# Kernel tuning notes

Hardware: AMD Instinct MI355X
Metric: run time of the kernel (lower is better)

The kernel has to match this reference:

```python
import jax, jax.numpy as jnp
import numpy as np

H = 56; W = 56; WS = 7; SHIFT = 3; HEADS = 4; C = 128; B = 64
N = WS * WS            # 49 tokens per window
NW = (H // WS) * (W // WS)  # 64 windows per image
HD = C // HEADS
EPS = 1e-5


def _rel_index():
    # matches get_relative_index: pairwise coord diffs in [-(WS-1), WS-1];
    # torch negative indexing wraps, so take mod (2*WS-1)
    coords = np.array([[i, j] for i in range(WS) for j in range(WS)])
    rel = coords[None, :, :] - coords[:, None, :]          # (N, N, 2)
    return (rel % (2 * WS - 1)).astype(np.int32)


def _attn_mask():
    # matches get_attn_mask for shifted windows
    img = np.zeros((H, W))
    sl = (slice(0, -WS), slice(-WS, -SHIFT), slice(-SHIFT, None))
    cnt = 0
    for hs in sl:
        for ws_ in sl:
            img[hs, ws_] = cnt
            cnt += 1
    m = img.reshape(H // WS, WS, W // WS, WS).transpose(0, 2, 1, 3).reshape(NW, N)
    am = m[:, None, :] - m[:, :, None]                     # (NW, N, N)
    return np.where(am != 0, -100.0, 0.0).astype(np.float32)

_REL_IDX = _rel_index()
_MASK = _attn_mask()


def _layernorm(x, g, b):
    mu = jnp.mean(x, axis=-1, keepdims=True)
    var = jnp.mean(jnp.square(x - mu), axis=-1, keepdims=True)
    return (x - mu) * jax.lax.rsqrt(var + EPS) * g + b


def setup_inputs() -> dict:
    key = jax.random.key(0)
    ks = jax.random.split(key, 16)
    s = 0.02
    return {
        "x": jax.random.normal(ks[0], (B, H * W, C), jnp.float32),
        "wq": jax.random.normal(ks[1], (C, C), jnp.float32) * s,
        "bq": jnp.zeros((C,), jnp.float32),
        "wk": jax.random.normal(ks[2], (C, C), jnp.float32) * s,
        "bk": jnp.zeros((C,), jnp.float32),
        "wv": jax.random.normal(ks[3], (C, C), jnp.float32) * s,
        "bv": jnp.zeros((C,), jnp.float32),
        "wo": jax.random.normal(ks[4], (C, C), jnp.float32) * s,
        "bo": jnp.zeros((C,), jnp.float32),
        "rel_table": jax.random.normal(ks[5], (2 * WS - 1, 2 * WS - 1, HEADS), jnp.float32) * s,
        "ln1_g": jnp.ones((C,), jnp.float32),
        "ln1_b": jnp.zeros((C,), jnp.float32),
        "ln2_g": jnp.ones((C,), jnp.float32),
        "ln2_b": jnp.zeros((C,), jnp.float32),
        "w1": jax.random.normal(ks[6], (C, 4 * C), jnp.float32) * s,
        "b1": jnp.zeros((4 * C,), jnp.float32),
        "w2": jax.random.normal(ks[7], (4 * C, C), jnp.float32) * s,
        "b2": jnp.zeros((C,), jnp.float32),
    }


def reference(x, wq, bq, wk, bk, wv, bv, wo, bo, rel_table,
              ln1_g, ln1_b, ln2_g, ln2_b, w1, b1, w2, b2):
    shortcut = x                                     # (B, H*W, C)
    h = _layernorm(x, ln1_g, ln1_b).reshape(B, H, W, C)
    h = jnp.roll(h, (-SHIFT, -SHIFT), axis=(1, 2))   # cyclic shift
    # window partition -> (B*NW, N, C)
    h = h.reshape(B, H // WS, WS, W // WS, WS, C).transpose(0, 1, 3, 2, 4, 5)
    h = h.reshape(B * NW, N, C)
    q = (h @ wq + bq).reshape(B * NW, N, HEADS, HD)
    k = (h @ wk + bk).reshape(B * NW, N, HEADS, HD)
    v = (h @ wv + bv).reshape(B * NW, N, HEADS, HD)
    attn = jnp.einsum('nqhd,nkhd->nhqk', q, k) / np.sqrt(HD).astype(np.float32)
    bias = rel_table[_REL_IDX[:, :, 0], _REL_IDX[:, :, 1]]  # (N, N, HEADS)
    attn = attn + jnp.transpose(bias, (2, 0, 1))[None]      # (1, H, N, N)
    # shifted-window additive mask
    attn = attn.reshape(B, NW, HEADS, N, N) + jnp.asarray(_MASK)[None, :, None]
    attn = jax.nn.softmax(attn.reshape(B * NW, HEADS, N, N), axis=-1)
    out = jnp.einsum('nhqk,nkhd->nqhd', attn, v).reshape(B * NW, N, C)
    out = out @ wo + bo
    # faithful to source bug: output taken directly from window-ordered tokens
    h = out.reshape(B, H * W, C)
    h = h + shortcut
    m = _layernorm(h, ln2_g, ln2_b)
    m = jax.nn.gelu(m @ w1 + b1, approximate=False) @ w2 + b2
    return h + m
```

## Files before the change

### kernel.cpp

```cpp
#include <hip/hip_runtime.h>

typedef __attribute__((ext_vector_type(8))) short short8;
typedef __attribute__((ext_vector_type(4))) float f32x4;
typedef unsigned short u16;
typedef unsigned int u32;

#define MFMA16(a, b, c) __builtin_amdgcn_mfma_f32_16x16x32_bf16((a), (b), (c), 0, 0, 0)
#define SCALE_Q 0.1767766952966369f
#define TOKENS 200704

__device__ __forceinline__ u16 f2bf(float x) {
  u32 u = __float_as_uint(x);
  u32 r = u + 0x7FFF + ((u >> 16) & 1);
  return (u16)(r >> 16);
}

__device__ __forceinline__ float gelu_f(float x) {
  float u = 0.7978845608f * (x + 0.044715f * x * x * x);
  float e = __expf(2.f * u);
  float t = 1.f - 2.f / (e + 1.f);
  return 0.5f * x * (1.f + t);
}

__device__ __forceinline__ u32 pairpack(u16 me, int lane) {
  u32 pv = (u32)__shfl_xor((int)me, 1);
  return (u32)me | (pv << 16);
}

__global__ __launch_bounds__(256) void k0_weights(
    const float* __restrict__ wq, const float* __restrict__ wk, const float* __restrict__ wv,
    const float* __restrict__ wo, const float* __restrict__ w1, const float* __restrict__ w2,
    const float* __restrict__ bq, const float* __restrict__ bk, const float* __restrict__ bv,
    u16* __restrict__ wqkvt, u16* __restrict__ wot, u16* __restrict__ w1t, u16* __restrict__ w2t,
    float* __restrict__ bqkv) {
  int idx = blockIdx.x * 256 + threadIdx.x;
  if (idx < 49152) {
    int n = idx >> 7, k = idx & 127;
    float v;
    if (n < 128) v = wq[k * 128 + n] * SCALE_Q;
    else if (n < 256) v = wk[k * 128 + (n - 128)];
    else v = wv[k * 128 + (n - 256)];
    wqkvt[idx] = f2bf(v);
  } else if (idx < 65536) {
    int j = idx - 49152;
    int n = j >> 7, k = j & 127;
    wot[j] = f2bf(wo[k * 128 + n]);
  } else if (idx < 131072) {
    int j = idx - 65536;
    int n = j >> 7, k = j & 127;
    w1t[j] = f2bf(w1[k * 512 + n]);
  } else if (idx < 196608) {
    int j = idx - 131072;
    int n = j >> 9, k = j & 511;
    w2t[j] = f2bf(w2[k * 128 + n]);
  } else if (idx < 196992) {
    int n = idx - 196608;
    float v;
    if (n < 128) v = bq[n] * SCALE_Q;
    else if (n < 256) v = bk[n - 128];
    else v = bv[n - 256];
    bqkv[n] = v;
  }
}

__global__ __launch_bounds__(256) void k0_biasmask(const float* __restrict__ rel, float* __restrict__ bm) {
  int idx = blockIdx.x * 256 + threadIdx.x;
  int reg = idx & 3;
  int lane = (idx >> 2) & 63;
  int nt = (idx >> 8) & 3;
  int mt = (idx >> 10) & 3;
  int h = (idx >> 12) & 3;
  int wi = idx >> 14;
  int r = mt * 16 + ((lane >> 4) << 2) + reg;
  int c = nt * 16 + (lane & 15);
  float v = -1e30f;
  if (r < 49 && c < 49) {
    int qr = r / 7, qc = r % 7, kr = c / 7, kc = c % 7;
    int i0 = (kr - qr + 13) % 13, i1 = (kc - qc + 13) % 13;
    v = rel[(i0 * 13 + i1) * 4 + h];
    int gh = (wi >> 3) * 7 + qr, gw = (wi & 7) * 7 + qc;
    int kh = (wi >> 3) * 7 + kr, kw = (wi & 7) * 7 + kc;
    int rq = (gh < 49 ? 0 : (gh < 53 ? 1 : 2)) * 3 + (gw < 49 ? 0 : (gw < 53 ? 1 : 2));
    int rk = (kh < 49 ? 0 : (kh < 53 ? 1 : 2)) * 3 + (kw < 49 ? 0 : (kw < 53 ? 1 : 2));
    if (rq != rk) v -= 100.f;
  }
  bm[idx] = v;
}

__global__ __launch_bounds__(256) void k1_ln1(const float* __restrict__ x, const float* __restrict__ g,
                                              const float* __restrict__ b, u16* __restrict__ hwin) {
  int wid = threadIdx.x >> 6, lane = threadIdx.x & 63;
  int t = blockIdx.x * 4 + wid;
  float2 v = *(const float2*)(x + (size_t)t * 128 + lane * 2);
  float s = v.x + v.y;
#pragma unroll
  for (int o = 1; o < 64; o <<= 1) s += __shfl_xor(s, o);
  float mu = s * 0.0078125f;
  float dx = v.x - mu, dy = v.y - mu;
  float q = dx * dx + dy * dy;
#pragma unroll
  for (int o = 1; o < 64; o <<= 1) q += __shfl_xor(q, o);
  float rstd = rsqrtf(q * 0.0078125f + 1e-5f);
  float y0 = dx * rstd * g[lane * 2] + b[lane * 2];
  float y1 = dy * rstd * g[lane * 2 + 1] + b[lane * 2 + 1];
  int bi = t / 3136, hw = t - bi * 3136;
  int oh = hw / 56, ow = hw - oh * 56;
  int gh = oh - 3; if (gh < 0) gh += 56;
  int gw = ow - 3; if (gw < 0) gw += 56;
  int win = bi * 64 + (gh / 7) * 8 + gw / 7;
  int n = (gh % 7) * 7 + (gw % 7);
  u32 packed = (u32)f2bf(y0) | ((u32)f2bf(y1) << 16);
  *(u32*)(hwin + (size_t)(win * 49 + n) * 128 + lane * 2) = packed;
}

__global__ __launch_bounds__(256) void k2_qkv(const u16* __restrict__ hwin, const u16* __restrict__ wt,
                                              const float* __restrict__ bqkv, u16* __restrict__ qb,
                                              u16* __restrict__ kb, u16* __restrict__ vb) {
  int tid = threadIdx.x, lane = tid & 63, w = tid >> 6;
  int g = lane >> 4, l15 = lane & 15;
  int row0 = blockIdx.x * 128 + w * 32;
  short8 a[2][4];
#pragma unroll
  for (int mt = 0; mt < 2; ++mt)
#pragma unroll
    for (int kt = 0; kt < 4; ++kt)
      a[mt][kt] = *(const short8*)(hwin + (size_t)(row0 + mt * 16 + l15) * 128 + kt * 32 + g * 8);
  const f32x4 vz = {0.f, 0.f, 0.f, 0.f};
  for (int nb = 0; nb < 6; ++nb) {
    f32x4 acc[2][4];
#pragma unroll
    for (int i = 0; i < 2; ++i)
#pragma unroll
      for (int j = 0; j < 4; ++j) acc[i][j] = vz;
#pragma unroll
    for (int kt = 0; kt < 4; ++kt) {
      short8 bfr[4];
#pragma unroll
      for (int nt = 0; nt < 4; ++nt)
        bfr[nt] = *(const short8*)(wt + (size_t)(nb * 64 + nt * 16 + l15) * 128 + kt * 32 + g * 8);
#pragma unroll
      for (int mt = 0; mt < 2; ++mt)
#pragma unroll
        for (int nt = 0; nt < 4; ++nt) acc[mt][nt] = MFMA16(a[mt][kt], bfr[nt], acc[mt][nt]);
    }
    u16* dst; int cb;
    if (nb < 2) { dst = qb; cb = nb * 64; }
    else if (nb < 4) { dst = kb; cb = (nb - 2) * 64; }
    else { dst = vb; cb = (nb - 4) * 64; }
#pragma unroll
    for (int mt = 0; mt < 2; ++mt)
#pragma unroll
      for (int nt = 0; nt < 4; ++nt) {
        int c = cb + nt * 16 + l15;
        float bias = bqkv[nb * 64 + nt * 16 + l15];
#pragma unroll
        for (int reg = 0; reg < 4; ++reg) {
          int token = row0 + mt * 16 + g * 4 + reg;
          u16 me = f2bf(acc[mt][nt][reg] + bias);
          u32 word = pairpack(me, lane);
          if (!(lane & 1)) *(u32*)(dst + (size_t)token * 128 + c) = word;
        }
      }
  }
}

__global__ __launch_bounds__(256) void k3_attn(const u16* __restrict__ qb, const u16* __restrict__ kb,
                                               const u16* __restrict__ vb, const float* __restrict__ bm,
                                               const u16* __restrict__ wot, const float* __restrict__ bo,
                                               const float* __restrict__ x, const float* __restrict__ g2,
                                               const float* __restrict__ b2, float* __restrict__ dout,
                                               u16* __restrict__ ln2) {
  __shared__ u16 smem[16384 + 8192];
  u16* pl = smem;
  u16* vtl = smem + 16384;
  u16* aol = smem;
  int win = blockIdx.x;
  int tid = threadIdx.x;
  int lane = tid & 63, head = tid >> 6;
  int g = lane >> 4, l15 = lane & 15;

  {
    int t = tid >> 2, dq = tid & 3;
    long grow = (long)win * 49 + t;
    bool valid = (t < 49) && (grow < TOKENS);
    short8 r[4];
#pragma unroll
    for (int c = 0; c < 4; ++c) {
      if (valid) r[c] = *(const short8*)(vb + grow * 128 + dq * 32 + c * 8);
      else r[c] = short8{0, 0, 0, 0, 0, 0, 0, 0};
    }
#pragma unroll
    for (int c = 0; c < 4; ++c)
#pragma unroll
      for (int e = 0; e < 8; ++e) {
        int d = dq * 32 + c * 8 + e;
        int byte_ = (d * 128 + t * 2) ^ ((((d & 7) ^ ((d >> 3) & 7))) << 4);
        *(u16*)((char*)vtl + byte_) = (u16)r[c][e];
      }
  }

  u16* myp = pl + head * 4096;
  short8 aq[4], bk_[4];
#pragma unroll
  for (int mt = 0; mt < 4; ++mt)
    aq[mt] = *(const short8*)(qb + (size_t)(win * 49 + mt * 16 + l15) * 128 + head * 32 + g * 8);
#pragma unroll
  for (int nt = 0; nt < 4; ++nt)
    bk_[nt] = *(const short8*)(kb + (size_t)(win * 49 + nt * 16 + l15) * 128 + head * 32 + g * 8);
  const f32x4* bmv = (const f32x4*)bm + ((win & 63) * 4 + head) * 1024;
  f32x4 s[4][4];
#pragma unroll
  for (int mt = 0; mt < 4; ++mt)
#pragma unroll
    for (int nt = 0; nt < 4; ++nt) s[mt][nt] = bmv[(mt * 4 + nt) * 64 + lane];
#pragma unroll
  for (int mt = 0; mt < 4; ++mt)
#pragma unroll
    for (int nt = 0; nt < 4; ++nt) s[mt][nt] = MFMA16(aq[mt], bk_[nt], s[mt][nt]);
#pragma unroll
  for (int mt = 0; mt < 4; ++mt)
#pragma unroll
    for (int reg = 0; reg < 4; ++reg) {
      float m = fmaxf(fmaxf(s[mt][0][reg], s[mt][1][reg]), fmaxf(s[mt][2][reg], s[mt][3][reg]));
#pragma unroll
      for (int o = 1; o < 16; o <<= 1) m = fmaxf(m, __shfl_xor(m, o));
      float p0 = __expf(s[mt][0][reg] - m);
      float p1 = __expf(s[mt][1][reg] - m);
      float p2 = __expf(s[mt][2][reg] - m);
      float p3 = __expf(s[mt][3][reg] - m);
      float sum = p0 + p1 + p2 + p3;
#pragma unroll
      for (int o = 1; o < 16; o <<= 1) sum += __shfl_xor(sum, o);
      float rinv = 1.f / sum;
      s[mt][0][reg] = p0 * rinv; s[mt][1][reg] = p1 * rinv;
      s[mt][2][reg] = p2 * rinv; s[mt][3][reg] = p3 * rinv;
    }
#pragma unroll
  for (int mt = 0; mt < 4; ++mt)
#pragma unroll
    for (int nt = 0; nt < 4; ++nt)
#pragma unroll
      for (int reg = 0; reg < 4; ++reg) {
        int r = mt * 16 + g * 4 + reg, c = nt * 16 + l15;
        int byte_ = ((r << 7) + (c << 1)) ^ ((r & 7) << 4);
        *(u16*)((char*)myp + byte_) = f2bf(s[mt][nt][reg]);
      }
  __syncthreads();

  short8 vf[2][2];
#pragma unroll
  for (int kk = 0; kk < 2; ++kk)
#pragma unroll
    for (int n2 = 0; n2 < 2; ++n2) {
      int d = head * 32 + n2 * 16 + l15;
      int byte_ = (d * 128 + (kk * 32 + g * 8) * 2) ^ ((((d & 7) ^ ((d >> 3) & 7))) << 4);
      vf[kk][n2] = *(const short8*)((const char*)vtl + byte_);
    }
  const f32x4 vz = {0.f, 0.f, 0.f, 0.f};
  f32x4 o[4][2];
#pragma unroll
  for (int mt = 0; mt < 4; ++mt) { o[mt][0] = vz; o[mt][1] = vz; }
#pragma unroll
  for (int mt = 0; mt < 4; ++mt)
#pragma unroll
    for (int kk = 0; kk < 2; ++kk) {
      int r = mt * 16 + l15;
      int byte_ = ((r << 7) + kk * 64 + g * 16) ^ ((r & 7) << 4);
      short8 pa = *(const short8*)((const char*)myp + byte_);
#pragma unroll
      for (int n2 = 0; n2 < 2; ++n2) o[mt][n2] = MFMA16(pa, vf[kk][n2], o[mt][n2]);
    }
  __syncthreads();

#pragma unroll
  for (int mt = 0; mt < 4; ++mt)
#pragma unroll
    for (int n2 = 0; n2 < 2; ++n2)
#pragma unroll
      for (int reg = 0; reg < 4; ++reg) {
        int r = mt * 16 + g * 4 + reg, c = head * 32 + n2 * 16 + l15;
        u16 me = f2bf(o[mt][n2][reg]);
        u32 word = pairpack(me, lane);
        if (!(lane & 1)) {
          int byte_ = ((r << 8) + c * 2) ^ ((r & 7) << 4);
          *(u32*)((char*)aol + byte_) = word;
        }
      }
  __syncthreads();

  int w = head;
  f32x4 pacc[8];
#pragma unroll
  for (int nt = 0; nt < 8; ++nt) pacc[nt] = vz;
#pragma unroll
  for (int kt = 0; kt < 4; ++kt) {
    int row = w * 16 + l15;
    int byte_ = ((row << 8) + kt * 64 + g * 16) ^ ((row & 7) << 4);
    short8 af = *(const short8*)((const char*)aol + byte_);
#pragma unroll
    for (int nt = 0; nt < 8; ++nt) {
      short8 bf = *(const short8*)(wot + (size_t)(nt * 16 + l15) * 128 + kt * 32 + g * 8);
      pacc[nt] = MFMA16(af, bf, pacc[nt]);
    }
  }
#pragma unroll
  for (int reg = 0; reg < 4; ++reg) {
    int row = w * 16 + g * 4 + reg;
    if (row < 49) {
      size_t token = (size_t)win * 49 + row;
      float hv[8];
      float s1 = 0.f, s2 = 0.f;
#pragma unroll
      for (int nt = 0; nt < 8; ++nt) {
        int c = nt * 16 + l15;
        float v = pacc[nt][reg] + bo[c] + x[token * 128 + c];
        dout[token * 128 + c] = v;
        hv[nt] = v; s1 += v; s2 += v * v;
      }
#pragma unroll
      for (int o = 1; o < 16; o <<= 1) { s1 += __shfl_xor(s1, o); s2 += __shfl_xor(s2, o); }
      float mu = s1 * 0.0078125f;
      float rstd = rsqrtf(fmaxf(s2 * 0.0078125f - mu * mu, 0.f) + 1e-5f);
#pragma unroll
      for (int nt = 0; nt < 8; ++nt) {
        int c = nt * 16 + l15;
        u16 me = f2bf((hv[nt] - mu) * rstd * g2[c] + b2[c]);
        u32 word = pairpack(me, lane);
        if (!(lane & 1)) *(u32*)(ln2 + token * 128 + c) = word;
      }
    }
  }
}

__global__ __launch_bounds__(256) void k5_mlp(const u16* __restrict__ ln2, const u16* __restrict__ w1t,
                                              const float* __restrict__ b1, const u16* __restrict__ w2t,
                                              const float* __restrict__ b2, float* __restrict__ dout) {
  __shared__ u16 h1[64 * 512];
  int tid = threadIdx.x, lane = tid & 63, w = tid >> 6;
  int g = lane >> 4, l15 = lane & 15;
  int row0 = blockIdx.x * 64;
  const f32x4 vz = {0.f, 0.f, 0.f, 0.f};

  {
    int r0 = w * 16;
    short8 a[4];
#pragma unroll
    for (int kt = 0; kt < 4; ++kt)
      a[kt] = *(const short8*)(ln2 + (size_t)(row0 + r0 + l15) * 128 + kt * 32 + g * 8);
    for (int nb = 0; nb < 8; ++nb) {
      f32x4 acc[4];
#pragma unroll
      for (int j = 0; j < 4; ++j) acc[j] = vz;
#pragma unroll
      for (int kt = 0; kt < 4; ++kt) {
        short8 bf[4];
#pragma unroll
        for (int nt = 0; nt < 4; ++nt)
          bf[nt] = *(const short8*)(w1t + (size_t)(nb * 64 + nt * 16 + l15) * 128 + kt * 32 + g * 8);
#pragma unroll
        for (int nt = 0; nt < 4; ++nt) acc[nt] = MFMA16(a[kt], bf[nt], acc[nt]);
      }
#pragma unroll
      for (int nt = 0; nt < 4; ++nt) {
        float bias = b1[nb * 64 + nt * 16 + l15];
#pragma unroll
        for (int reg = 0; reg < 4; ++reg) {
          int r = r0 + g * 4 + reg;
          int c = nb * 64 + nt * 16 + l15;
          u16 me = f2bf(gelu_f(acc[nt][reg] + bias));
          u32 word = pairpack(me, lane);
          if (!(lane & 1)) {
            int byte_ = (r * 1024 + c * 2) ^ ((r & 7) << 4);
            *(u32*)((char*)h1 + byte_) = word;
          }
        }
      }
    }
  }
  __syncthreads();

  {
    int c0 = w * 32;
    f32x4 acc2[4][2];
#pragma unroll
    for (int i = 0; i < 4; ++i) { acc2[i][0] = vz; acc2[i][1] = vz; }
#pragma unroll
    for (int kt = 0; kt < 16; ++kt) {
      short8 bf[2];
#pragma unroll
      for (int n2 = 0; n2 < 2; ++n2)
        bf[n2] = *(const short8*)(w2t + (size_t)(c0 + n2 * 16 + l15) * 512 + kt * 32 + g * 8);
#pragma unroll
      for (int mt = 0; mt < 4; ++mt) {
        int r = mt * 16 + l15;
        int byte_ = (r * 1024 + kt * 64 + g * 16) ^ ((r & 7) << 4);
        short8 af = *(const short8*)((const char*)h1 + byte_);
#pragma unroll
        for (int n2 = 0; n2 < 2; ++n2) acc2[mt][n2] = MFMA16(af, bf[n2], acc2[mt][n2]);
      }
    }
#pragma unroll
    for (int mt = 0; mt < 4; ++mt)
#pragma unroll
      for (int n2 = 0; n2 < 2; ++n2) {
        int c = c0 + n2 * 16 + l15;
        float bias = b2[c];
#pragma unroll
        for (int reg = 0; reg < 4; ++reg) {
          size_t token = (size_t)row0 + mt * 16 + g * 4 + reg;
          size_t i = token * 128 + c;
          dout[i] = acc2[mt][n2][reg] + bias + dout[i];
        }
      }
  }
}

extern "C" void kernel_launch(void* const* d_in, const int* in_sizes, int n_in,
                              void* d_out, int out_size, void* d_ws, size_t ws_size,
                              hipStream_t stream) {
  const float* x    = (const float*)d_in[0];
  const float* wq   = (const float*)d_in[1];
  const float* bq   = (const float*)d_in[2];
  const float* wk   = (const float*)d_in[3];
  const float* bk   = (const float*)d_in[4];
  const float* wv   = (const float*)d_in[5];
  const float* bv   = (const float*)d_in[6];
  const float* wo   = (const float*)d_in[7];
  const float* bo   = (const float*)d_in[8];
  const float* rel  = (const float*)d_in[9];
  const float* ln1g = (const float*)d_in[10];
  const float* ln1b = (const float*)d_in[11];
  const float* ln2g = (const float*)d_in[12];
  const float* ln2b = (const float*)d_in[13];
  const float* w1   = (const float*)d_in[14];
  const float* b1   = (const float*)d_in[15];
  const float* w2   = (const float*)d_in[16];
  const float* b2   = (const float*)d_in[17];
  float* out = (float*)d_out;
  char* ws = (char*)d_ws;

  float* bmask = (float*)(ws);
  u16* wqkvt = (u16*)(ws + (size_t)(4 << 20));
  u16* wot   = (u16*)(ws + (size_t)(4 << 20) + 196608);
  u16* w1t   = (u16*)(ws + (size_t)(4 << 20) + 229376);
  u16* w2t   = (u16*)(ws + (size_t)(4 << 20) + 360448);
  float* bqkv = (float*)(ws + (size_t)(4 << 20) + 491520);
  const size_t SB = (size_t)TOKENS * 128 * 2;
  u16* hwin = (u16*)(ws + (size_t)(8 << 20));
  u16* qb   = (u16*)(ws + (size_t)(8 << 20) + SB);
  u16* kb   = (u16*)(ws + (size_t)(8 << 20) + 2 * SB);
  u16* vb   = (u16*)(ws + (size_t)(8 << 20) + 3 * SB);
  u16* ln2  = hwin;

  k0_weights<<<770, 256, 0, stream>>>(wq, wk, wv, wo, w1, w2, bq, bk, bv,
                                      wqkvt, wot, w1t, w2t, bqkv);
  k0_biasmask<<<4096, 256, 0, stream>>>(rel, bmask);
  k1_ln1<<<50176, 256, 0, stream>>>(x, ln1g, ln1b, hwin);
  k2_qkv<<<1568, 256, 0, stream>>>(hwin, wqkvt, bqkv, qb, kb, vb);
  k3_attn<<<4096, 256, 0, stream>>>(qb, kb, vb, bmask, wot, bo, x, ln2g, ln2b, out, ln2);
  k5_mlp<<<3136, 256, 0, stream>>>(ln2, w1t, b1, w2t, b2, out);
}
```

Baseline: 884.3 us.

## Halve per-block rows in QKV and MLP kernels, store bf16 directly to LDS

The QKV projection now gives each wave 16 rows instead of 32 and launches twice as many blocks. The MLP kernel handles 32 rows per block, splitting the hidden columns across wave pairs, which halves its shared-memory tile and doubles the grid. Shared-memory epilogue writes in attention and MLP replace the shuffle-based pair packing with plain 16-bit stores. This aims to cut registers and LDS per block for higher occupancy and fewer shuffles, at the cost of more weight reloads per token and narrower LDS writes.

```diff
diff --git a/kernel.cpp b/kernel.cpp
--- a/kernel.cpp
+++ b/kernel.cpp
@@ -118,20 +118,16 @@
                                               u16* __restrict__ kb, u16* __restrict__ vb) {
   int tid = threadIdx.x, lane = tid & 63, w = tid >> 6;
   int g = lane >> 4, l15 = lane & 15;
-  int row0 = blockIdx.x * 128 + w * 32;
-  short8 a[2][4];
-#pragma unroll
-  for (int mt = 0; mt < 2; ++mt)
-#pragma unroll
-    for (int kt = 0; kt < 4; ++kt)
-      a[mt][kt] = *(const short8*)(hwin + (size_t)(row0 + mt * 16 + l15) * 128 + kt * 32 + g * 8);
+  int row0 = blockIdx.x * 64 + w * 16;
+  short8 a[4];
+#pragma unroll
+  for (int kt = 0; kt < 4; ++kt)
+    a[kt] = *(const short8*)(hwin + (size_t)(row0 + l15) * 128 + kt * 32 + g * 8);
   const f32x4 vz = {0.f, 0.f, 0.f, 0.f};
   for (int nb = 0; nb < 6; ++nb) {
-    f32x4 acc[2][4];
-#pragma unroll
-    for (int i = 0; i < 2; ++i)
-#pragma unroll
-      for (int j = 0; j < 4; ++j) acc[i][j] = vz;
+    f32x4 acc[4];
+#pragma unroll
+    for (int j = 0; j < 4; ++j) acc[j] = vz;
 #pragma unroll
     for (int kt = 0; kt < 4; ++kt) {
       short8 bfr[4];
@@ -139,28 +135,24 @@
       for (int nt = 0; nt < 4; ++nt)
         bfr[nt] = *(const short8*)(wt + (size_t)(nb * 64 + nt * 16 + l15) * 128 + kt * 32 + g * 8);
 #pragma unroll
-      for (int mt = 0; mt < 2; ++mt)
-#pragma unroll
-        for (int nt = 0; nt < 4; ++nt) acc[mt][nt] = MFMA16(a[mt][kt], bfr[nt], acc[mt][nt]);
+      for (int nt = 0; nt < 4; ++nt) acc[nt] = MFMA16(a[kt], bfr[nt], acc[nt]);
     }
     u16* dst; int cb;
     if (nb < 2) { dst = qb; cb = nb * 64; }
     else if (nb < 4) { dst = kb; cb = (nb - 2) * 64; }
     else { dst = vb; cb = (nb - 4) * 64; }
 #pragma unroll
-    for (int mt = 0; mt < 2; ++mt)
-#pragma unroll
-      for (int nt = 0; nt < 4; ++nt) {
-        int c = cb + nt * 16 + l15;
-        float bias = bqkv[nb * 64 + nt * 16 + l15];
-#pragma unroll
-        for (int reg = 0; reg < 4; ++reg) {
-          int token = row0 + mt * 16 + g * 4 + reg;
-          u16 me = f2bf(acc[mt][nt][reg] + bias);
-          u32 word = pairpack(me, lane);
-          if (!(lane & 1)) *(u32*)(dst + (size_t)token * 128 + c) = word;
-        }
-      }
+    for (int nt = 0; nt < 4; ++nt) {
+      int c = cb + nt * 16 + l15;
+      float bias = bqkv[nb * 64 + nt * 16 + l15];
+#pragma unroll
+      for (int reg = 0; reg < 4; ++reg) {
+        int token = row0 + g * 4 + reg;
+        u16 me = f2bf(acc[nt][reg] + bias);
+        u32 word = pairpack(me, lane);
+        if (!(lane & 1)) *(u32*)(dst + (size_t)token * 128 + c) = word;
+      }
+    }
   }
 }
 
@@ -279,12 +271,8 @@
 #pragma unroll
       for (int reg = 0; reg < 4; ++reg) {
         int r = mt * 16 + g * 4 + reg, c = head * 32 + n2 * 16 + l15;
-        u16 me = f2bf(o[mt][n2][reg]);
-        u32 word = pairpack(me, lane);
-        if (!(lane & 1)) {
-          int byte_ = ((r << 8) + c * 2) ^ ((r & 7) << 4);
-          *(u32*)((char*)aol + byte_) = word;
-        }
+        int byte_ = ((r << 8) + c * 2) ^ ((r & 7) << 4);
+        *(u16*)((char*)aol + byte_) = f2bf(o[mt][n2][reg]);
       }
   __syncthreads();
 
@@ -335,19 +323,20 @@
 __global__ __launch_bounds__(256) void k5_mlp(const u16* __restrict__ ln2, const u16* __restrict__ w1t,
                                               const float* __restrict__ b1, const u16* __restrict__ w2t,
                                               const float* __restrict__ b2, float* __restrict__ dout) {
-  __shared__ u16 h1[64 * 512];
+  __shared__ u16 h1[32 * 512];
   int tid = threadIdx.x, lane = tid & 63, w = tid >> 6;
   int g = lane >> 4, l15 = lane & 15;
-  int row0 = blockIdx.x * 64;
+  int row0 = blockIdx.x * 32;
   const f32x4 vz = {0.f, 0.f, 0.f, 0.f};
 
   {
-    int r0 = w * 16;
+    int r0 = (w & 1) * 16, c0 = (w >> 1) * 256;
     short8 a[4];
 #pragma unroll
     for (int kt = 0; kt < 4; ++kt)
       a[kt] = *(const short8*)(ln2 + (size_t)(row0 + r0 + l15) * 128 + kt * 32 + g * 8);
-    for (int nb = 0; nb < 8; ++nb) {
+#pragma unroll
+    for (int nb = 0; nb < 4; ++nb) {
       f32x4 acc[4];
 #pragma unroll
       for (int j = 0; j < 4; ++j) acc[j] = vz;
@@ -356,23 +345,20 @@
         short8 bf[4];
 #pragma unroll
         for (int nt = 0; nt < 4; ++nt)
-          bf[nt] = *(const short8*)(w1t + (size_t)(nb * 64 + nt * 16 + l15) * 128 + kt * 32 + g * 8);
+          bf[nt] = *(const short8*)(w1t + (size_t)(c0 + nb * 64 + nt * 16 + l15) * 128 + kt * 32 + g * 8);
 #pragma unroll
         for (int nt = 0; nt < 4; ++nt) acc[nt] = MFMA16(a[kt], bf[nt], acc[nt]);
       }
 #pragma unroll
       for (int nt = 0; nt < 4; ++nt) {
-        float bias = b1[nb * 64 + nt * 16 + l15];
+        int c = c0 + nb * 64 + nt * 16 + l15;
+        float bias = b1[c];
 #pragma unroll
         for (int reg = 0; reg < 4; ++reg) {
           int r = r0 + g * 4 + reg;
-          int c = nb * 64 + nt * 16 + l15;
           u16 me = f2bf(gelu_f(acc[nt][reg] + bias));
-          u32 word = pairpack(me, lane);
-          if (!(lane & 1)) {
-            int byte_ = (r * 1024 + c * 2) ^ ((r & 7) << 4);
-            *(u32*)((char*)h1 + byte_) = word;
-          }
+          int byte_ = (r * 1024 + c * 2) ^ ((r & 7) << 4);
+          *(u16*)((char*)h1 + byte_) = me;
         }
       }
     }
@@ -381,9 +367,9 @@
 
   {
     int c0 = w * 32;
-    f32x4 acc2[4][2];
-#pragma unroll
-    for (int i = 0; i < 4; ++i) { acc2[i][0] = vz; acc2[i][1] = vz; }
+    f32x4 acc2[2][2];
+#pragma unroll
+    for (int i = 0; i < 2; ++i) { acc2[i][0] = vz; acc2[i][1] = vz; }
 #pragma unroll
     for (int kt = 0; kt < 16; ++kt) {
       short8 bf[2];
@@ -391,7 +377,7 @@
       for (int n2 = 0; n2 < 2; ++n2)
         bf[n2] = *(const short8*)(w2t + (size_t)(c0 + n2 * 16 + l15) * 512 + kt * 32 + g * 8);
 #pragma unroll
-      for (int mt = 0; mt < 4; ++mt) {
+      for (int mt = 0; mt < 2; ++mt) {
         int r = mt * 16 + l15;
         int byte_ = (r * 1024 + kt * 64 + g * 16) ^ ((r & 7) << 4);
         short8 af = *(const short8*)((const char*)h1 + byte_);
@@ -400,7 +386,7 @@
       }
     }
 #pragma unroll
-    for (int mt = 0; mt < 4; ++mt)
+    for (int mt = 0; mt < 2; ++mt)
 #pragma unroll
       for (int n2 = 0; n2 < 2; ++n2) {
         int c = c0 + n2 * 16 + l15;
@@ -456,7 +442,7 @@
                                       wqkvt, wot, w1t, w2t, bqkv);
   k0_biasmask<<<4096, 256, 0, stream>>>(rel, bmask);
   k1_ln1<<<50176, 256, 0, stream>>>(x, ln1g, ln1b, hwin);
-  k2_qkv<<<1568, 256, 0, stream>>>(hwin, wqkvt, bqkv, qb, kb, vb);
+  k2_qkv<<<3136, 256, 0, stream>>>(hwin, wqkvt, bqkv, qb, kb, vb);
   k3_attn<<<4096, 256, 0, stream>>>(qb, kb, vb, bmask, wot, bo, x, ln2g, ln2b, out, ln2);
-  k5_mlp<<<3136, 256, 0, stream>>>(ln2, w1t, b1, w2t, b2, out);
-}
+  k5_mlp<<<6272, 256, 0, stream>>>(ln2, w1t, b1, w2t, b2, out);
+}
```

After: 887.2 us. Within noise of the previous version (+0.3%).
